# Kernel optimization log

Hardware: AMD Instinct MI355X
Metric: run time of the kernel (lower is better)

## Reference

```python
import jax, jax.numpy as jnp
import numpy as np
from jax import lax

DIM = 192
HEADS = 8
B, H, W = 8, 128, 128


def dwconv3x3(x, w):
    # x: [B,C,H,W], w: [C,1,3,3] depthwise (groups=C)
    return lax.conv_general_dilated(
        x, w, window_strides=(1, 1), padding='SAME',
        feature_group_count=x.shape[1],
        dimension_numbers=('NCHW', 'OIHW', 'NCHW'))


def conv1x1(x, w, b=None):
    # w: [Cout, Cin]
    y = jnp.einsum('oc,bchw->bohw', w, x)
    if b is not None:
        y = y + b[None, :, None, None]
    return y


def setup_inputs() -> dict:
    key = jax.random.key(0)
    ks = jax.random.split(key, 9)
    s = 0.02
    return {
        'x': jax.random.normal(ks[0], (B, DIM, H, W), jnp.float32),
        'w_qkv': jax.random.normal(ks[1], (3 * DIM, DIM), jnp.float32) * s,
        'b_qkv': jnp.zeros((3 * DIM,), jnp.float32),
        'w_dw': jax.random.normal(ks[2], (3 * DIM, 1, 3, 3), jnp.float32) * s,
        'b_dw': jnp.zeros((3 * DIM,), jnp.float32),
        'w_proj': jax.random.normal(ks[3], (DIM, DIM), jnp.float32) * s,
        'b_proj': jnp.zeros((DIM,), jnp.float32),
        'w_pos1': jax.random.normal(ks[4], (DIM, 1, 3, 3), jnp.float32) * s,
        'w_pos2': jax.random.normal(ks[5], (DIM, 1, 3, 3), jnp.float32) * s,
        'temperature': jnp.ones((HEADS, 1, 1), jnp.float32),
    }


def reference(x, w_qkv, b_qkv, w_dw, b_dw, w_proj, b_proj, w_pos1, w_pos2, temperature):
    b, c, h, w = x.shape
    heads = HEADS
    ch = c // heads

    qkv = conv1x1(x, w_qkv, b_qkv)
    qkv = dwconv3x3(qkv, w_dw) + b_dw[None, :, None, None]
    q_inp, k_inp, v_inp = jnp.split(qkv, 3, axis=1)

    def to_heads(t):  # [B,C,H,W] -> [B,heads,ch,HW]
        return t.reshape(b, heads, ch, h * w)

    q = to_heads(q_inp)
    k = to_heads(k_inp)
    v = to_heads(v_inp)

    # L2 normalize over hw (torch F.normalize, eps=1e-12)
    q = q / jnp.maximum(jnp.linalg.norm(q, axis=-1, keepdims=True), 1e-12)
    k = k / jnp.maximum(jnp.linalg.norm(k, axis=-1, keepdims=True), 1e-12)

    attn = jnp.einsum('bhce,bhde->bhcd', q, k) * temperature  # [B,heads,ch,ch]
    attn = jax.nn.softmax(attn, axis=-1)
    out = jnp.einsum('bhcd,bhde->bhce', attn, v)  # [B,heads,ch,HW]
    out = out.reshape(b, c, h, w)

    out = conv1x1(out, w_proj, b_proj)

    pos = dwconv3x3(v_inp, w_pos1)
    pos = jax.nn.gelu(pos, approximate=False)
    pos = dwconv3x3(pos, w_pos2)

    return out + pos
```

## Files before the change

### kernel.cpp

```cpp
#include <hip/hip_runtime.h>
#include <stdint.h>
#include <stddef.h>

#define NB 8
#define CC 192
#define C3 576
#define HGT 128
#define WID 128
#define HW 16384
#define NH 8

typedef short bf16x8 __attribute__((ext_vector_type(8)));
typedef float f32x4 __attribute__((ext_vector_type(4)));

__device__ __forceinline__ unsigned short f2bf(float f) {
  unsigned int u = __float_as_uint(f);
  u += 0x7fffu + ((u >> 16) & 1u);
  return (unsigned short)(u >> 16);
}
__device__ __forceinline__ float bf2f(unsigned short h) {
  return __uint_as_float(((unsigned int)h) << 16);
}
__device__ __forceinline__ unsigned int pk2(float a, float b) {
  return (unsigned int)f2bf(a) | ((unsigned int)f2bf(b) << 16);
}
__device__ __forceinline__ void gl_lds16(const void* g, void* l) {
  __builtin_amdgcn_global_load_lds(
      (const __attribute__((address_space(1))) unsigned int*)(uintptr_t)g,
      (__attribute__((address_space(3))) unsigned int*)(uint32_t)(uintptr_t)l,
      16, 0, 0);
}
__device__ __forceinline__ int xcd_swz(int g, int n) {
  return (g & 7) * (n >> 3) + (g >> 3);
}

__global__ __launch_bounds__(256) void ktrans(const float* __restrict__ x,
                                              unsigned char* __restrict__ xT) {
  __shared__ __align__(16) float lx[192 * 68];
  int wg = xcd_swz(blockIdx.x, gridDim.x);
  int pt = wg & 255, b = wg >> 8;
  int p0 = pt * 64;
  int tid = threadIdx.x;
#pragma unroll
  for (int i = 0; i < 12; ++i) {
    int f = tid + i * 256;
    int ic = f >> 4, q = f & 15;
    float4 v = *(const float4*)(x + ((size_t)(b * CC + ic)) * HW + p0 + q * 4);
    *(float4*)(lx + ic * 68 + q * 4) = v;
  }
  __syncthreads();
#pragma unroll
  for (int i = 0; i < 6; ++i) {
    int f = i * 256 + tid;
    int s = f >> 6, p = f & 63;
    unsigned int wv[4];
#pragma unroll
    for (int j = 0; j < 4; ++j)
      wv[j] = pk2(lx[(s * 8 + 2 * j) * 68 + p], lx[(s * 8 + 2 * j + 1) * 68 + p]);
    uint4 st; st.x = wv[0]; st.y = wv[1]; st.z = wv[2]; st.w = wv[3];
    *(uint4*)(xT + (((size_t)(b * 24 + s)) * HW + p0 + p) * 16) = st;
  }
}

__global__ void kwprep(const float* __restrict__ wq, unsigned char* __restrict__ wb) {
  int f = blockIdx.x * 256 + threadIdx.x;
  if (f >= C3 * 24) return;
  int oc = f / 24, s = f % 24;
  unsigned int wv[4];
#pragma unroll
  for (int j = 0; j < 4; ++j)
    wv[j] = pk2(wq[oc * 192 + s * 8 + 2 * j], wq[oc * 192 + s * 8 + 2 * j + 1]);
  uint4 st; st.x = wv[0]; st.y = wv[1]; st.z = wv[2]; st.w = wv[3];
  *(uint4*)(wb + (size_t)oc * 384 + ((s ^ (oc & 7)) * 16)) = st;
}

__global__ __launch_bounds__(256) void kconv1(const unsigned char* __restrict__ xT,
                                              const unsigned char* __restrict__ wb,
                                              const float* __restrict__ bqkv,
                                              unsigned short* __restrict__ t) {
  __shared__ __align__(16) unsigned char lds[73728];
  int wg = xcd_swz(blockIdx.x, gridDim.x);
  int ot = wg % 9;
  int pt = (wg / 9) & 127;
  int b = wg / 1152;
  int tid = threadIdx.x;
  const unsigned char* gB = wb + (size_t)ot * 64 * 384;
#pragma unroll
  for (int i = 0; i < 12; ++i) {
    int u2 = i * 256 + tid;
    int slot = u2 >> 7, px = u2 & 127;
    gl_lds16(xT + (((size_t)(b * 24 + slot)) * HW + pt * 128 + px) * 16, lds + u2 * 16);
  }
#pragma unroll
  for (int i = 0; i < 6; ++i)
    gl_lds16(gB + i * 4096 + tid * 16, lds + 49152 + i * 4096 + tid * 16);
  asm volatile("s_waitcnt vmcnt(0)" ::: "memory");
  __syncthreads();

  int lane = tid & 63, wv = tid >> 6;
  int l15 = lane & 15, gq = lane >> 4;
  int pw = (wv >> 1) * 64, ow = (wv & 1) * 32;
  f32x4 acc[4][2];
#pragma unroll
  for (int a = 0; a < 4; ++a)
#pragma unroll
    for (int c = 0; c < 2; ++c) acc[a][c] = (f32x4){0.f, 0.f, 0.f, 0.f};

#pragma unroll
  for (int kk = 0; kk < 6; ++kk) {
    int cb = kk * 64 + gq * 16;
    bf16x8 af[4], bfr[2];
#pragma unroll
    for (int mf = 0; mf < 4; ++mf)
      af[mf] = *(const bf16x8*)(lds + (((kk * 4 + gq) << 7) + pw + mf * 16 + l15) * 16);
#pragma unroll
    for (int nf = 0; nf < 2; ++nf) {
      int r = ow + nf * 16 + l15;
      bfr[nf] = *(const bf16x8*)(lds + 49152 + r * 384 + (cb ^ ((r & 7) << 4)));
    }
#pragma unroll
    for (int mf = 0; mf < 4; ++mf)
#pragma unroll
      for (int nf = 0; nf < 2; ++nf)
        acc[mf][nf] = __builtin_amdgcn_mfma_f32_16x16x32_bf16(af[mf], bfr[nf], acc[mf][nf], 0, 0, 0);
  }
#pragma unroll
  for (int nf = 0; nf < 2; ++nf) {
    int oc = ot * 64 + ow + nf * 16 + l15;
    float bias = bqkv[oc];
    int part = oc / 192, c = oc % 192;
    size_t rowb = ((size_t)((part * 8 + b) * CC + c)) * HW;
#pragma unroll
    for (int mf = 0; mf < 4; ++mf) {
      int p = pt * 128 + pw + mf * 16 + gq * 4;
      uint2 st;
      st.x = pk2(acc[mf][nf][0] + bias, acc[mf][nf][1] + bias);
      st.y = pk2(acc[mf][nf][2] + bias, acc[mf][nf][3] + bias);
      *(uint2*)(t + rowb + p) = st;
    }
  }
}

__global__ __launch_bounds__(256) void kdw(const unsigned short* __restrict__ src,
                                           const float* __restrict__ wdw,
                                           const float* __restrict__ bdw,
                                           int part, int mode,
                                           unsigned short* __restrict__ dst,
                                           float* __restrict__ nrm,
                                           unsigned char* __restrict__ vT) {
  __shared__ __align__(16) unsigned int smem[8 * 721];
  int wg = xcd_swz(blockIdx.x, gridDim.x);
  int cg = wg % 24, rt = (wg / 24) & 15, b = wg / 384;
  int y0 = rt * 8, chg0 = cg * 8;
  int tid = threadIdx.x;
  for (int i = tid; i < 5768; i += 256) smem[i] = 0;
  __syncthreads();
#pragma unroll
  for (int i = 0; i < 5; ++i) {
    int f = i * 256 + tid;
    int ch = f / 160, rem = f % 160;
    int r = rem >> 4, seg = rem & 15;
    int y = y0 - 1 + r;
    if (y >= 0 && y < HGT) {
      uint4 v = *(const uint4*)(src + ((size_t)(b * CC + chg0 + ch)) * HW + y * WID + seg * 8);
      unsigned int* dp = smem + ch * 721 + r * 72 + 4 + seg * 4;
      dp[0] = v.x; dp[1] = v.y; dp[2] = v.z; dp[3] = v.w;
    }
  }
  __syncthreads();

  int ch = tid >> 5, u = tid & 31;
  int row = u >> 2, xs = (u & 3) * 32;
  int gch = part * CC + chg0 + ch;
  float wv[9];
#pragma unroll
  for (int j = 0; j < 9; ++j) wv[j] = wdw[gch * 9 + j];
  float bias = bdw[gch];
  float outv[32];
  const unsigned int* tb = smem + ch * 721;
#pragma unroll
  for (int g = 0; g < 4; ++g) {
    int x0 = xs + g * 8;
    float v[3][12];
#pragma unroll
    for (int dy = 0; dy < 3; ++dy) {
      const unsigned int* rp = tb + (row + dy) * 72 + ((x0 + 6) >> 1);
#pragma unroll
      for (int m = 0; m < 6; ++m) {
        unsigned int w2 = rp[m];
        v[dy][2 * m] = bf2f((unsigned short)(w2 & 0xffff));
        v[dy][2 * m + 1] = bf2f((unsigned short)(w2 >> 16));
      }
    }
#pragma unroll
    for (int j = 0; j < 8; ++j) {
      float a = bias;
#pragma unroll
      for (int dy = 0; dy < 3; ++dy)
#pragma unroll
        for (int dx = 0; dx < 3; ++dx)
          a += v[dy][j + dx + 1] * wv[dy * 3 + dx];
      outv[g * 8 + j] = a;
    }
  }

  if (mode == 0) {
    size_t rb = ((size_t)(b * CC + chg0 + ch)) * HW + (size_t)(y0 + row) * WID + xs;
#pragma unroll
    for (int g = 0; g < 4; ++g) {
      uint4 st;
      st.x = pk2(outv[g * 8 + 0], outv[g * 8 + 1]);
      st.y = pk2(outv[g * 8 + 2], outv[g * 8 + 3]);
      st.z = pk2(outv[g * 8 + 4], outv[g * 8 + 5]);
      st.w = pk2(outv[g * 8 + 6], outv[g * 8 + 7]);
      *(uint4*)(dst + rb + g * 8) = st;
    }
    float s = 0.f;
#pragma unroll
    for (int i = 0; i < 32; ++i) s += outv[i] * outv[i];
#pragma unroll
    for (int m = 16; m >= 1; m >>= 1) s += __shfl_xor(s, m, 32);
    if (u == 0) {
      int qc = chg0 + ch;
      atomicAdd(nrm + (b * NH + qc / 24) * 24 + (qc % 24), s);
    }
  } else {
    __syncthreads();
    unsigned short* vt = (unsigned short*)smem;
#pragma unroll
    for (int g = 0; g < 4; ++g)
#pragma unroll
      for (int j = 0; j < 8; j += 2) {
        int x = xs + g * 8 + j;
        ((unsigned int*)smem)[ch * 512 + row * 64 + (x >> 1)] =
            pk2(outv[g * 8 + j], outv[g * 8 + j + 1]);
      }
    __syncthreads();
#pragma unroll
    for (int i = 0; i < 4; ++i) {
      int f = i * 256 + tid;
      int r = f >> 7, col = f & 127;
      unsigned int wvp[4];
#pragma unroll
      for (int e = 0; e < 4; ++e) {
        unsigned short a = vt[(2 * e) * 1024 + r * 128 + col];
        unsigned short bb = vt[(2 * e + 1) * 1024 + r * 128 + col];
        wvp[e] = (unsigned int)a | ((unsigned int)bb << 16);
      }
      uint4 st; st.x = wvp[0]; st.y = wvp[1]; st.z = wvp[2]; st.w = wvp[3];
      *(uint4*)(vT + (((size_t)(b * 24 + cg)) * HW + (size_t)(y0 + r) * WID + col) * 16) = st;
    }
  }
}

__global__ __launch_bounds__(256) void kgram(const unsigned short* __restrict__ q,
                                             const unsigned short* __restrict__ k,
                                             float* __restrict__ G) {
  __shared__ __align__(16) unsigned char qt[32768];
  __shared__ __align__(16) unsigned char kt[32768];
  __shared__ float gpart[4][32][32];
  int blk = blockIdx.x;
  int b = blk >> 5, h = (blk >> 2) & 7, qr = blk & 3;
  int tid = threadIdx.x, lane = tid & 63, w = tid >> 6;
  int l15 = lane & 15, gq = lane >> 4;
  for (int i = tid; i < 2048; i += 256) {
    ((unsigned int*)(qt + 24576))[i] = 0;
    ((unsigned int*)(kt + 24576))[i] = 0;
  }
  f32x4 acc[2][2];
#pragma unroll
  for (int a = 0; a < 2; ++a)
#pragma unroll
    for (int d = 0; d < 2; ++d) acc[a][d] = (f32x4){0.f, 0.f, 0.f, 0.f};
  for (int c = 0; c < 8; ++c) {
    __syncthreads();
    int px0 = qr * 4096 + c * 512;
#pragma unroll
    for (int i = 0; i < 6; ++i) {
      int f = i * 256 + tid;
      int rowc = f >> 6, seg = f & 63;
      size_t gofs = ((size_t)(b * CC + h * 24 + rowc)) * HW + px0 + seg * 8;
      unsigned int lofs = rowc * 1024 + ((seg * 16) ^ ((rowc & 7) << 4));
      *(uint4*)(qt + lofs) = *(const uint4*)(q + gofs);
      *(uint4*)(kt + lofs) = *(const uint4*)(k + gofs);
    }
    __syncthreads();
#pragma unroll
    for (int j = 0; j < 4; ++j) {
      int kk = w * 4 + j;
      int cb = kk * 64 + gq * 16;
      bf16x8 aq[2], bk[2];
#pragma unroll
      for (int ct = 0; ct < 2; ++ct) {
        int r = ct * 16 + l15;
        aq[ct] = *(const bf16x8*)(qt + r * 1024 + (cb ^ ((r & 7) << 4)));
        bk[ct] = *(const bf16x8*)(kt + r * 1024 + (cb ^ ((r & 7) << 4)));
      }
#pragma unroll
      for (int ct = 0; ct < 2; ++ct)
#pragma unroll
        for (int dt = 0; dt < 2; ++dt)
          acc[ct][dt] = __builtin_amdgcn_mfma_f32_16x16x32_bf16(aq[ct], bk[dt], acc[ct][dt], 0, 0, 0);
    }
  }
  __syncthreads();
#pragma unroll
  for (int ct = 0; ct < 2; ++ct)
#pragma unroll
    for (int dt = 0; dt < 2; ++dt)
#pragma unroll
      for (int r = 0; r < 4; ++r)
        gpart[w][ct * 16 + gq * 4 + r][dt * 16 + l15] = acc[ct][dt][r];
  __syncthreads();
  for (int f = tid; f < 576; f += 256) {
    int cc2 = f / 24, d = f % 24;
    float s = gpart[0][cc2][d] + gpart[1][cc2][d] + gpart[2][cc2][d] + gpart[3][cc2][d];
    atomicAdd(G + ((size_t)(b * NH + h)) * 576 + cc2 * 24 + d, s);
  }
}

__global__ __launch_bounds__(256) void kattn(const float* __restrict__ G,
                                             const float* __restrict__ nq,
                                             const float* __restrict__ nk,
                                             const float* __restrict__ temp,
                                             const float* __restrict__ wproj,
                                             unsigned char* __restrict__ W2) {
  __shared__ float attn[24][24];
  __shared__ float iq[24], ik[24];
  int bh = blockIdx.x;
  int h = bh & 7, b = bh >> 3;
  int tid = threadIdx.x;
  const float* Gb = G + (size_t)bh * 576;
  if (tid < 24) { float n = sqrtf(nq[bh * 24 + tid]); iq[tid] = 1.f / fmaxf(n, 1e-12f); }
  else if (tid < 48) { float n = sqrtf(nk[bh * 24 + tid - 24]); ik[tid - 24] = 1.f / fmaxf(n, 1e-12f); }
  __syncthreads();
  if (tid < 24) {
    float tmp = temp[h];
    float row[24];
    float mx = -1e30f;
#pragma unroll
    for (int d = 0; d < 24; ++d) {
      row[d] = Gb[tid * 24 + d] * iq[tid] * ik[d] * tmp;
      mx = fmaxf(mx, row[d]);
    }
    float sum = 0.f;
#pragma unroll
    for (int d = 0; d < 24; ++d) { float e = expf(row[d] - mx); row[d] = e; sum += e; }
    float inv = 1.f / sum;
#pragma unroll
    for (int d = 0; d < 24; ++d) attn[tid][d] = row[d] * inv;
  }
  __syncthreads();
  for (int i = 0; i < 18; ++i) {
    int f = tid + i * 256;
    if (f >= 4608) break;
    int oc = f / 24, d = f % 24;
    float s = 0.f;
#pragma unroll
    for (int c = 0; c < 24; ++c) s += wproj[oc * 192 + h * 24 + c] * attn[c][d];
    int gg = h * 24 + d;
    *(unsigned short*)(W2 + ((size_t)b * CC + oc) * 384 + ((gg * 2) ^ ((oc & 7) << 4))) = f2bf(s);
  }
}

__global__ __launch_bounds__(256) void kpos(const unsigned char* __restrict__ vT,
                                            const float* __restrict__ w1,
                                            const float* __restrict__ w2,
                                            unsigned short* __restrict__ pos) {
  __shared__ unsigned int vbuf[8 * 865];
  __shared__ unsigned int d1[8 * 721];
  int wg = xcd_swz(blockIdx.x, gridDim.x);
  int cg = wg % 24, rt = (wg / 24) & 15, b = wg / 384;
  int y0 = rt * 8, g0 = cg * 8;
  int tid = threadIdx.x;
  for (int i = tid; i < 6920; i += 256) vbuf[i] = 0;
  __syncthreads();
#pragma unroll
  for (int i = 0; i < 3; ++i) {
    int f = i * 256 + tid;
    int r = f >> 6, colp = f & 63;
    int y = y0 - 2 + r;
    if (y >= 0 && y < HGT) {
      const unsigned char* base = vT + (((size_t)(b * 24 + cg)) * HW + (size_t)y * WID + colp * 2) * 16;
      uint4 va = *(const uint4*)(base);
      uint4 vb2 = *(const uint4*)(base + 16);
      unsigned int la[4] = {va.x, va.y, va.z, va.w};
      unsigned int lb[4] = {vb2.x, vb2.y, vb2.z, vb2.w};
#pragma unroll
      for (int e = 0; e < 8; ++e) {
        unsigned int a16 = (la[e >> 1] >> ((e & 1) * 16)) & 0xffff;
        unsigned int b16 = (lb[e >> 1] >> ((e & 1) * 16)) & 0xffff;
        vbuf[e * 865 + r * 72 + colp + 4] = a16 | (b16 << 16);
      }
    }
  }
  __syncthreads();
  int ch = tid >> 5, u = tid & 31;
  {
    const float* wp = w1 + (g0 + ch) * 9;
    float wl[9];
#pragma unroll
    for (int j = 0; j < 9; ++j) wl[j] = wp[j];
    int x0 = u * 4;
    for (int rr = 0; rr < 10; ++rr) {
      int y = y0 - 1 + rr;
      unsigned int o0 = 0, o1 = 0;
      if (y >= 0 && y < HGT) {
        float v[3][8];
#pragma unroll
        for (int dy = 0; dy < 3; ++dy) {
          const unsigned int* rp = vbuf + ch * 865 + (rr + dy) * 72 + ((x0 + 6) >> 1);
#pragma unroll
          for (int m = 0; m < 4; ++m) {
            unsigned int w2r = rp[m];
            v[dy][2 * m] = bf2f((unsigned short)(w2r & 0xffff));
            v[dy][2 * m + 1] = bf2f((unsigned short)(w2r >> 16));
          }
        }
        float g4[4];
#pragma unroll
        for (int j = 0; j < 4; ++j) {
          float a = 0.f;
#pragma unroll
          for (int dy = 0; dy < 3; ++dy)
#pragma unroll
            for (int dx = 0; dx < 3; ++dx)
              a += v[dy][j + dx + 1] * wl[dy * 3 + dx];
          g4[j] = 0.5f * a * (1.f + erff(a * 0.70710678118f));
        }
        o0 = pk2(g4[0], g4[1]);
        o1 = pk2(g4[2], g4[3]);
      }
      unsigned int* dp = d1 + ch * 721 + rr * 72 + ((x0 + 8) >> 1);
      dp[0] = o0; dp[1] = o1;
    }
  }
  if (tid < 160) {
    int ech = tid / 20, rem = tid % 20;
    int rr = rem >> 1, side = rem & 1;
    int x = side ? 128 : -1;
    int y = y0 - 1 + rr;
    unsigned short val = 0;
    if (y >= 0 && y < HGT) {
      const float* wp = w1 + (g0 + ech) * 9;
      float a = 0.f;
      const unsigned short* vb16 = (const unsigned short*)(vbuf + ech * 865);
#pragma unroll
      for (int dy = 0; dy < 3; ++dy)
#pragma unroll
        for (int dx = 0; dx < 3; ++dx)
          a += bf2f(vb16[(rr + dy) * 144 + (x + dx + 7)]) * wp[dy * 3 + dx];
      val = f2bf(0.5f * a * (1.f + erff(a * 0.70710678118f)));
    }
    ((unsigned short*)(d1 + ech * 721))[rr * 144 + (x + 8)] = val;
  }
  __syncthreads();
  {
    const float* wp = w2 + (g0 + ch) * 9;
    float wl[9];
#pragma unroll
    for (int j = 0; j < 9; ++j) wl[j] = wp[j];
    int row = u >> 2, xs = (u & 3) * 32;
    size_t rb = ((size_t)(b * CC + g0 + ch)) * HW + (size_t)(y0 + row) * WID;
#pragma unroll
    for (int g = 0; g < 4; ++g) {
      int x0 = xs + g * 8;
      float v[3][12];
#pragma unroll
      for (int dy = 0; dy < 3; ++dy) {
        const unsigned int* rp = d1 + ch * 721 + (row + dy) * 72 + ((x0 + 6) >> 1);
#pragma unroll
        for (int m = 0; m < 6; ++m) {
          unsigned int w2r = rp[m];
          v[dy][2 * m] = bf2f((unsigned short)(w2r & 0xffff));
          v[dy][2 * m + 1] = bf2f((unsigned short)(w2r >> 16));
        }
      }
      uint4 st;
      float o[8];
#pragma unroll
      for (int j = 0; j < 8; ++j) {
        float a = 0.f;
#pragma unroll
        for (int dy = 0; dy < 3; ++dy)
#pragma unroll
          for (int dx = 0; dx < 3; ++dx)
            a += v[dy][j + dx + 1] * wl[dy * 3 + dx];
        o[j] = a;
      }
      st.x = pk2(o[0], o[1]); st.y = pk2(o[2], o[3]);
      st.z = pk2(o[4], o[5]); st.w = pk2(o[6], o[7]);
      *(uint4*)(pos + rb + x0) = st;
    }
  }
}

__global__ __launch_bounds__(256) void kproj(const unsigned char* __restrict__ vT,
                                             const unsigned char* __restrict__ W2,
                                             const float* __restrict__ bproj,
                                             const unsigned short* __restrict__ pos,
                                             float* __restrict__ out) {
  __shared__ __align__(16) unsigned char lds[73728];
  int wg = xcd_swz(blockIdx.x, gridDim.x);
  int ot = wg % 3;
  int pt = (wg / 3) & 127;
  int b = wg / 384;
  int tid = threadIdx.x;
  const unsigned char* gB = W2 + ((size_t)(b * CC + ot * 64)) * 384;
#pragma unroll
  for (int i = 0; i < 12; ++i) {
    int u2 = i * 256 + tid;
    int slot = u2 >> 7, px = u2 & 127;
    gl_lds16(vT + (((size_t)(b * 24 + slot)) * HW + pt * 128 + px) * 16, lds + u2 * 16);
  }
#pragma unroll
  for (int i = 0; i < 6; ++i)
    gl_lds16(gB + i * 4096 + tid * 16, lds + 49152 + i * 4096 + tid * 16);
  asm volatile("s_waitcnt vmcnt(0)" ::: "memory");
  __syncthreads();

  int lane = tid & 63, wv = tid >> 6;
  int l15 = lane & 15, gq = lane >> 4;
  int pw = (wv >> 1) * 64, ow = (wv & 1) * 32;
  f32x4 acc[4][2];
#pragma unroll
  for (int a = 0; a < 4; ++a)
#pragma unroll
    for (int c = 0; c < 2; ++c) acc[a][c] = (f32x4){0.f, 0.f, 0.f, 0.f};

#pragma unroll
  for (int kk = 0; kk < 6; ++kk) {
    int cb = kk * 64 + gq * 16;
    bf16x8 af[4], bfr[2];
#pragma unroll
    for (int mf = 0; mf < 4; ++mf)
      af[mf] = *(const bf16x8*)(lds + (((kk * 4 + gq) << 7) + pw + mf * 16 + l15) * 16);
#pragma unroll
    for (int nf = 0; nf < 2; ++nf) {
      int r = ow + nf * 16 + l15;
      bfr[nf] = *(const bf16x8*)(lds + 49152 + r * 384 + (cb ^ ((r & 7) << 4)));
    }
#pragma unroll
    for (int mf = 0; mf < 4; ++mf)
#pragma unroll
      for (int nf = 0; nf < 2; ++nf)
        acc[mf][nf] = __builtin_amdgcn_mfma_f32_16x16x32_bf16(af[mf], bfr[nf], acc[mf][nf], 0, 0, 0);
  }
#pragma unroll
  for (int nf = 0; nf < 2; ++nf) {
    int oc = ot * 64 + ow + nf * 16 + l15;
    float bias = bproj[oc];
    size_t rowb = ((size_t)(b * CC + oc)) * HW;
#pragma unroll
    for (int mf = 0; mf < 4; ++mf) {
      int p = pt * 128 + pw + mf * 16 + gq * 4;
      uint2 pv = *(const uint2*)(pos + rowb + p);
      float4 o;
      o.x = acc[mf][nf][0] + bias + bf2f((unsigned short)(pv.x & 0xffff));
      o.y = acc[mf][nf][1] + bias + bf2f((unsigned short)(pv.x >> 16));
      o.z = acc[mf][nf][2] + bias + bf2f((unsigned short)(pv.y & 0xffff));
      o.w = acc[mf][nf][3] + bias + bf2f((unsigned short)(pv.y >> 16));
      *(float4*)(out + rowb + p) = o;
    }
  }
}

#define OFF_W   ((size_t)0)
#define OFF_G   ((size_t)221184)
#define OFF_NQ  ((size_t)368640)
#define OFF_NK  ((size_t)374784)
#define OFF_W2  ((size_t)380928)
#define OFF_T   ((size_t)970752)
#define OFF_XT  ((size_t)151965696)

#define PART_ELEMS ((size_t)8 * CC * HW)

extern "C" void kernel_launch(void* const* d_in, const int* in_sizes, int n_in,
                              void* d_out, int out_size, void* d_ws, size_t ws_size,
                              hipStream_t stream) {
  const float* x     = (const float*)d_in[0];
  const float* wqkv  = (const float*)d_in[1];
  const float* bqkv  = (const float*)d_in[2];
  const float* wdw   = (const float*)d_in[3];
  const float* bdw   = (const float*)d_in[4];
  const float* wproj = (const float*)d_in[5];
  const float* bproj = (const float*)d_in[6];
  const float* wpos1 = (const float*)d_in[7];
  const float* wpos2 = (const float*)d_in[8];
  const float* temp  = (const float*)d_in[9];
  unsigned char* ws = (unsigned char*)d_ws;
  unsigned short* t = (unsigned short*)(ws + OFF_T);

  hipMemsetAsync(ws + OFF_G, 0, 147456 + 6144 + 6144, stream);
  kwprep<<<54, 256, 0, stream>>>(wqkv, ws + OFF_W);
  ktrans<<<2048, 256, 0, stream>>>(x, ws + OFF_XT);
  kconv1<<<9216, 256, 0, stream>>>(ws + OFF_XT, ws + OFF_W, bqkv, t);
  kdw<<<3072, 256, 0, stream>>>(t + 2 * PART_ELEMS, wdw, bdw, 2, 1,
                                nullptr, nullptr, ws + OFF_XT);
  kdw<<<3072, 256, 0, stream>>>(t, wdw, bdw, 0, 0,
                                t + 2 * PART_ELEMS, (float*)(ws + OFF_NQ), nullptr);
  kdw<<<3072, 256, 0, stream>>>(t + PART_ELEMS, wdw, bdw, 1, 0,
                                t, (float*)(ws + OFF_NK), nullptr);
  kgram<<<256, 256, 0, stream>>>(t + 2 * PART_ELEMS, t, (float*)(ws + OFF_G));
  kattn<<<64, 256, 0, stream>>>((const float*)(ws + OFF_G), (const float*)(ws + OFF_NQ),
                                (const float*)(ws + OFF_NK), temp, wproj, ws + OFF_W2);
  kpos<<<3072, 256, 0, stream>>>(ws + OFF_XT, wpos1, wpos2, t + PART_ELEMS);
  kproj<<<3072, 256, 0, stream>>>(ws + OFF_XT, ws + OFF_W2, bproj,
                                  t + PART_ELEMS, (float*)d_out);
}
```

Before: 352.0 us.

## Fuse q/k depthwise conv with Gram computation and pipeline the 1x1 GEMMs

The qkv 1x1 conv now writes q and k in a head-blocked, channel-interleaved layout. A new kernel fuses the q/k depthwise 3x3, the L2-norm accumulation and the q·k^T Gram MFMA, so the two intermediate q/k tensors no longer round-trip through memory. The v depthwise runs as its own kernel. Both the conv1 and proj GEMM kernels now loop over four 64-pixel tiles with double-buffered LDS prefetch and reuse the weights, using half as many blocks. The cost is heavier per-block work in the fused kernel, with redundant halo loads and atomics on G.

```diff
diff --git a/kernel.cpp b/kernel.cpp
--- a/kernel.cpp
+++ b/kernel.cpp
@@ -77,77 +77,251 @@
 __global__ __launch_bounds__(256) void kconv1(const unsigned char* __restrict__ xT,
                                               const unsigned char* __restrict__ wb,
                                               const float* __restrict__ bqkv,
-                                              unsigned short* __restrict__ t) {
+                                              unsigned short* __restrict__ vout,
+                                              unsigned char* __restrict__ qkout) {
   __shared__ __align__(16) unsigned char lds[73728];
   int wg = xcd_swz(blockIdx.x, gridDim.x);
-  int ot = wg % 9;
-  int pt = (wg / 9) & 127;
-  int b = wg / 1152;
+  int ot = wg % 9; int rest = wg / 9; int grp = rest & 63; int b = rest >> 6;
   int tid = threadIdx.x;
-  const unsigned char* gB = wb + (size_t)ot * 64 * 384;
-#pragma unroll
-  for (int i = 0; i < 12; ++i) {
-    int u2 = i * 256 + tid;
-    int slot = u2 >> 7, px = u2 & 127;
-    gl_lds16(xT + (((size_t)(b * 24 + slot)) * HW + pt * 128 + px) * 16, lds + u2 * 16);
-  }
+  const unsigned char* gB = wb + (size_t)ot * 24576;
 #pragma unroll
   for (int i = 0; i < 6; ++i)
     gl_lds16(gB + i * 4096 + tid * 16, lds + 49152 + i * 4096 + tid * 16);
-  asm volatile("s_waitcnt vmcnt(0)" ::: "memory");
-  __syncthreads();
-
-  int lane = tid & 63, wv = tid >> 6;
+  const unsigned char* gA = xT + (size_t)b * 24 * HW * 16;
+  int t0 = grp * 4;
+  {
+    int p0 = t0 * 64;
+#pragma unroll
+    for (int i = 0; i < 6; ++i) {
+      int f = i * 256 + tid;
+      gl_lds16(gA + (((size_t)(f >> 6)) * HW + p0 + (f & 63)) * 16, lds + f * 16);
+    }
+  }
+  int lane = tid & 63, w = tid >> 6;
   int l15 = lane & 15, gq = lane >> 4;
-  int pw = (wv >> 1) * 64, ow = (wv & 1) * 32;
-  f32x4 acc[4][2];
-#pragma unroll
-  for (int a = 0; a < 4; ++a)
-#pragma unroll
-    for (int c = 0; c < 2; ++c) acc[a][c] = (f32x4){0.f, 0.f, 0.f, 0.f};
-
-#pragma unroll
-  for (int kk = 0; kk < 6; ++kk) {
-    int cb = kk * 64 + gq * 16;
-    bf16x8 af[4], bfr[2];
-#pragma unroll
-    for (int mf = 0; mf < 4; ++mf)
-      af[mf] = *(const bf16x8*)(lds + (((kk * 4 + gq) << 7) + pw + mf * 16 + l15) * 16);
-#pragma unroll
-    for (int nf = 0; nf < 2; ++nf) {
-      int r = ow + nf * 16 + l15;
-      bfr[nf] = *(const bf16x8*)(lds + 49152 + r * 384 + (cb ^ ((r & 7) << 4)));
-    }
-#pragma unroll
-    for (int mf = 0; mf < 4; ++mf)
-#pragma unroll
-      for (int nf = 0; nf < 2; ++nf)
-        acc[mf][nf] = __builtin_amdgcn_mfma_f32_16x16x32_bf16(af[mf], bfr[nf], acc[mf][nf], 0, 0, 0);
-  }
-#pragma unroll
-  for (int nf = 0; nf < 2; ++nf) {
-    int oc = ot * 64 + ow + nf * 16 + l15;
-    float bias = bqkv[oc];
-    int part = oc / 192, c = oc % 192;
-    size_t rowb = ((size_t)((part * 8 + b) * CC + c)) * HW;
-#pragma unroll
-    for (int mf = 0; mf < 4; ++mf) {
-      int p = pt * 128 + pw + mf * 16 + gq * 4;
+  int pw = w * 16;
+  float bias[4];
+  size_t obase[4];
+  int isv[4];
+#pragma unroll
+  for (int nf = 0; nf < 4; ++nf) {
+    int oc = ot * 64 + nf * 16 + l15;
+    bias[nf] = bqkv[oc];
+    if (oc >= 384) {
+      isv[nf] = 1;
+      obase[nf] = ((size_t)(b * CC + oc - 384)) * HW * 2;
+    } else {
+      isv[nf] = 0;
+      int part = oc >= 192 ? 1 : 0;
+      int cm = oc - part * 192;
+      int h = cm / 24, ch = cm % 24;
+      obase[nf] = (size_t)(((part * 8 + b) * 8 + h) * 128) * 6144 + ch * 16 + (gq & 1) * 8;
+    }
+  }
+  for (int it = 0; it < 4; ++it) {
+    int tile = t0 + it;
+    asm volatile("s_waitcnt vmcnt(0)" ::: "memory");
+    __syncthreads();
+    int nb = it & 1;
+    if (it < 3) {
+      int p1 = (tile + 1) * 64;
+#pragma unroll
+      for (int i = 0; i < 6; ++i) {
+        int f = i * 256 + tid;
+        gl_lds16(gA + (((size_t)(f >> 6)) * HW + p1 + (f & 63)) * 16,
+                 lds + ((nb ^ 1) * 24576) + f * 16);
+      }
+    }
+    f32x4 acc[4];
+#pragma unroll
+    for (int nf = 0; nf < 4; ++nf) acc[nf] = (f32x4){0.f, 0.f, 0.f, 0.f};
+#pragma unroll
+    for (int kk = 0; kk < 6; ++kk) {
+      bf16x8 a = *(const bf16x8*)(lds + nb * 24576 + ((((kk * 4 + gq) << 6) + pw + l15) * 16));
+      int cb = kk * 64 + gq * 16;
+#pragma unroll
+      for (int nf = 0; nf < 4; ++nf) {
+        int r = nf * 16 + l15;
+        bf16x8 bfr = *(const bf16x8*)(lds + 49152 + r * 384 + (cb ^ ((r & 7) << 4)));
+        acc[nf] = __builtin_amdgcn_mfma_f32_16x16x32_bf16(a, bfr, acc[nf], 0, 0, 0);
+      }
+    }
+    int p = tile * 64 + pw + gq * 4;
+    int y = p >> 7, x = p & 127;
+#pragma unroll
+    for (int nf = 0; nf < 4; ++nf) {
       uint2 st;
-      st.x = pk2(acc[mf][nf][0] + bias, acc[mf][nf][1] + bias);
-      st.y = pk2(acc[mf][nf][2] + bias, acc[mf][nf][3] + bias);
-      *(uint2*)(t + rowb + p) = st;
-    }
-  }
-}
-
-__global__ __launch_bounds__(256) void kdw(const unsigned short* __restrict__ src,
+      st.x = pk2(acc[nf][0] + bias[nf], acc[nf][1] + bias[nf]);
+      st.y = pk2(acc[nf][2] + bias[nf], acc[nf][3] + bias[nf]);
+      if (isv[nf]) {
+        *(uint2*)((unsigned char*)vout + obase[nf] + (size_t)p * 2) = st;
+      } else {
+        *(uint2*)(qkout + obase[nf] + (size_t)y * 6144 + (x >> 3) * 384) = st;
+      }
+    }
+  }
+}
+
+__device__ __forceinline__ void dwoct(const unsigned char* lds, int t, int r0,
+                                      int xu, int ch, const float* w, float bias,
+                                      float* o) {
+#pragma unroll
+  for (int j = 0; j < 8; ++j) o[j] = bias;
+#pragma unroll
+  for (int dy = 0; dy < 3; ++dy) {
+    int ub = ((t * 6 + r0 + dy) * 16) * 24 + ch;
+    union { bf16x8 v; unsigned short s[8]; } m;
+    m.v = *(const bf16x8*)(lds + (size_t)(ub + xu * 24) * 16);
+    unsigned short lft = *(const unsigned short*)(lds + (size_t)(ub + (xu > 0 ? xu - 1 : 0) * 24) * 16 + 14);
+    unsigned short rgt = *(const unsigned short*)(lds + (size_t)(ub + (xu < 15 ? xu + 1 : 15) * 24) * 16);
+    float vwin[10];
+    vwin[0] = (xu > 0) ? bf2f(lft) : 0.f;
+    vwin[9] = (xu < 15) ? bf2f(rgt) : 0.f;
+#pragma unroll
+    for (int j = 0; j < 8; ++j) vwin[1 + j] = bf2f(m.s[j]);
+#pragma unroll
+    for (int j = 0; j < 8; ++j)
+      o[j] += vwin[j] * w[dy * 3] + vwin[j + 1] * w[dy * 3 + 1] + vwin[j + 2] * w[dy * 3 + 2];
+  }
+}
+
+__global__ __launch_bounds__(256) void kqk(const unsigned char* __restrict__ qk,
                                            const float* __restrict__ wdw,
                                            const float* __restrict__ bdw,
-                                           int part, int mode,
-                                           unsigned short* __restrict__ dst,
-                                           float* __restrict__ nrm,
-                                           unsigned char* __restrict__ vT) {
+                                           float* __restrict__ G,
+                                           float* __restrict__ nq,
+                                           float* __restrict__ nk) {
+  __shared__ __align__(16) unsigned char lds[73728];
+  int wg = xcd_swz(blockIdx.x, gridDim.x);
+  int band = wg & 31, bh = wg >> 5;
+  int h = bh & 7, b = bh >> 3;
+  int y0 = band * 4;
+  int tid = threadIdx.x;
+  if (band == 0 || band == 31) {
+#pragma unroll
+    for (int i = 0; i < 18; ++i)
+      *(uint4*)(lds + (i * 256 + tid) * 16) = (uint4){0, 0, 0, 0};
+    __syncthreads();
+  }
+#pragma unroll
+  for (int i = 0; i < 18; ++i) {
+    int f = i * 256 + tid;
+    int t = f / 2304, rem = f % 2304;
+    int r = rem / 384, u = rem % 384;
+    int y = y0 - 1 + r;
+    if (y >= 0 && y < HGT)
+      gl_lds16(qk + ((size_t)(((t * 8 + b) * 8 + h) * 128 + y)) * 6144 + u * 16,
+               lds + f * 16);
+  }
+  asm volatile("s_waitcnt vmcnt(0)" ::: "memory");
+  __syncthreads();
+
+  int lane = tid & 63, w = tid >> 6;
+  int l15 = lane & 15, gq = lane >> 4;
+  int ch0 = l15;
+  int ch1 = (l15 < 8) ? 16 + l15 : 23;
+  int c0 = h * 24 + ch0, c1 = h * 24 + ch1;
+  float wq0[9], wq1[9], wk0[9], wk1[9];
+#pragma unroll
+  for (int j = 0; j < 9; ++j) {
+    wq0[j] = wdw[c0 * 9 + j];        wq1[j] = wdw[c1 * 9 + j];
+    wk0[j] = wdw[(192 + c0) * 9 + j]; wk1[j] = wdw[(192 + c1) * 9 + j];
+  }
+  float bq0 = bdw[c0], bq1 = bdw[c1], bk0 = bdw[192 + c0], bk1 = bdw[192 + c1];
+
+  f32x4 acc[2][2];
+#pragma unroll
+  for (int ct = 0; ct < 2; ++ct)
+#pragma unroll
+    for (int dt = 0; dt < 2; ++dt) acc[ct][dt] = (f32x4){0.f, 0.f, 0.f, 0.f};
+  float nq0 = 0.f, nq1 = 0.f, nk0 = 0.f, nk1 = 0.f;
+
+#pragma unroll
+  for (int j4 = 0; j4 < 4; ++j4) {
+    int kt = w * 4 + j4;
+    int r0 = kt >> 2;
+    int xu = (kt & 3) * 4 + gq;
+    union { bf16x8 v; unsigned int u[4]; } fq0, fq1, fk0, fk1;
+    {
+      float o[8];
+      dwoct(lds, 0, r0, xu, ch0, wq0, bq0, o);
+#pragma unroll
+      for (int j = 0; j < 8; ++j) nq0 += o[j] * o[j];
+#pragma unroll
+      for (int e = 0; e < 4; ++e) fq0.u[e] = pk2(o[2 * e], o[2 * e + 1]);
+    }
+    {
+      float o[8];
+      dwoct(lds, 0, r0, xu, ch1, wq1, bq1, o);
+#pragma unroll
+      for (int j = 0; j < 8; ++j) nq1 += o[j] * o[j];
+#pragma unroll
+      for (int e = 0; e < 4; ++e) fq1.u[e] = pk2(o[2 * e], o[2 * e + 1]);
+    }
+    {
+      float o[8];
+      dwoct(lds, 1, r0, xu, ch0, wk0, bk0, o);
+#pragma unroll
+      for (int j = 0; j < 8; ++j) nk0 += o[j] * o[j];
+#pragma unroll
+      for (int e = 0; e < 4; ++e) fk0.u[e] = pk2(o[2 * e], o[2 * e + 1]);
+    }
+    {
+      float o[8];
+      dwoct(lds, 1, r0, xu, ch1, wk1, bk1, o);
+#pragma unroll
+      for (int j = 0; j < 8; ++j) nk1 += o[j] * o[j];
+#pragma unroll
+      for (int e = 0; e < 4; ++e) fk1.u[e] = pk2(o[2 * e], o[2 * e + 1]);
+    }
+    acc[0][0] = __builtin_amdgcn_mfma_f32_16x16x32_bf16(fq0.v, fk0.v, acc[0][0], 0, 0, 0);
+    acc[0][1] = __builtin_amdgcn_mfma_f32_16x16x32_bf16(fq0.v, fk1.v, acc[0][1], 0, 0, 0);
+    acc[1][0] = __builtin_amdgcn_mfma_f32_16x16x32_bf16(fq1.v, fk0.v, acc[1][0], 0, 0, 0);
+    acc[1][1] = __builtin_amdgcn_mfma_f32_16x16x32_bf16(fq1.v, fk1.v, acc[1][1], 0, 0, 0);
+  }
+  __syncthreads();
+  float* gp = (float*)lds;
+#pragma unroll
+  for (int ct = 0; ct < 2; ++ct)
+#pragma unroll
+    for (int dt = 0; dt < 2; ++dt)
+      *(f32x4*)(gp + (((w * 4 + ct * 2 + dt) * 64) + lane) * 4) = acc[ct][dt];
+  nq0 += __shfl_xor(nq0, 16); nq0 += __shfl_xor(nq0, 32);
+  nq1 += __shfl_xor(nq1, 16); nq1 += __shfl_xor(nq1, 32);
+  nk0 += __shfl_xor(nk0, 16); nk0 += __shfl_xor(nk0, 32);
+  nk1 += __shfl_xor(nk1, 16); nk1 += __shfl_xor(nk1, 32);
+  int nb24 = (b * NH + h) * 24;
+  if (lane < 16) {
+    atomicAdd(nq + nb24 + l15, nq0);
+    atomicAdd(nk + nb24 + l15, nk0);
+  }
+  if (lane < 8) {
+    atomicAdd(nq + nb24 + 16 + l15, nq1);
+    atomicAdd(nk + nb24 + 16 + l15, nk1);
+  }
+  __syncthreads();
+  float* Gb = G + (size_t)(b * NH + h) * 576;
+#pragma unroll
+  for (int ii = 0; ii < 3; ++ii) {
+    int f = ii * 256 + tid;
+    if (f < 576) {
+      int c = f / 24, d = f % 24;
+      int t4 = ((c >> 4) << 1) + (d >> 4);
+      int lane16 = (d & 15) + (((c & 15) >> 2) << 4);
+      int reg = c & 3;
+      float s = 0.f;
+#pragma unroll
+      for (int w4 = 0; w4 < 4; ++w4)
+        s += gp[((w4 * 4 + t4) * 64 + lane16) * 4 + reg];
+      atomicAdd(Gb + f, s);
+    }
+  }
+}
+
+__global__ __launch_bounds__(256) void kdwv(const unsigned short* __restrict__ src,
+                                            const float* __restrict__ wdw,
+                                            const float* __restrict__ bdw,
+                                            unsigned char* __restrict__ vT) {
   __shared__ __align__(16) unsigned int smem[8 * 721];
   int wg = xcd_swz(blockIdx.x, gridDim.x);
   int cg = wg % 24, rt = (wg / 24) & 15, b = wg / 384;
@@ -168,10 +342,9 @@
     }
   }
   __syncthreads();
-
   int ch = tid >> 5, u = tid & 31;
   int row = u >> 2, xs = (u & 3) * 32;
-  int gch = part * CC + chg0 + ch;
+  int gch = 384 + chg0 + ch;
   float wv[9];
 #pragma unroll
   for (int j = 0; j < 9; ++j) wv[j] = wdw[gch * 9 + j];
@@ -203,119 +376,30 @@
       outv[g * 8 + j] = a;
     }
   }
-
-  if (mode == 0) {
-    size_t rb = ((size_t)(b * CC + chg0 + ch)) * HW + (size_t)(y0 + row) * WID + xs;
-#pragma unroll
-    for (int g = 0; g < 4; ++g) {
-      uint4 st;
-      st.x = pk2(outv[g * 8 + 0], outv[g * 8 + 1]);
-      st.y = pk2(outv[g * 8 + 2], outv[g * 8 + 3]);
-      st.z = pk2(outv[g * 8 + 4], outv[g * 8 + 5]);
-      st.w = pk2(outv[g * 8 + 6], outv[g * 8 + 7]);
-      *(uint4*)(dst + rb + g * 8) = st;
-    }
-    float s = 0.f;
-#pragma unroll
-    for (int i = 0; i < 32; ++i) s += outv[i] * outv[i];
-#pragma unroll
-    for (int m = 16; m >= 1; m >>= 1) s += __shfl_xor(s, m, 32);
-    if (u == 0) {
-      int qc = chg0 + ch;
-      atomicAdd(nrm + (b * NH + qc / 24) * 24 + (qc % 24), s);
-    }
-  } else {
-    __syncthreads();
-    unsigned short* vt = (unsigned short*)smem;
-#pragma unroll
-    for (int g = 0; g < 4; ++g)
-#pragma unroll
-      for (int j = 0; j < 8; j += 2) {
-        int x = xs + g * 8 + j;
-        ((unsigned int*)smem)[ch * 512 + row * 64 + (x >> 1)] =
-            pk2(outv[g * 8 + j], outv[g * 8 + j + 1]);
-      }
-    __syncthreads();
-#pragma unroll
-    for (int i = 0; i < 4; ++i) {
-      int f = i * 256 + tid;
-      int r = f >> 7, col = f & 127;
-      unsigned int wvp[4];
-#pragma unroll
-      for (int e = 0; e < 4; ++e) {
-        unsigned short a = vt[(2 * e) * 1024 + r * 128 + col];
-        unsigned short bb = vt[(2 * e + 1) * 1024 + r * 128 + col];
-        wvp[e] = (unsigned int)a | ((unsigned int)bb << 16);
-      }
-      uint4 st; st.x = wvp[0]; st.y = wvp[1]; st.z = wvp[2]; st.w = wvp[3];
-      *(uint4*)(vT + (((size_t)(b * 24 + cg)) * HW + (size_t)(y0 + r) * WID + col) * 16) = st;
-    }
-  }
-}
-
-__global__ __launch_bounds__(256) void kgram(const unsigned short* __restrict__ q,
-                                             const unsigned short* __restrict__ k,
-                                             float* __restrict__ G) {
-  __shared__ __align__(16) unsigned char qt[32768];
-  __shared__ __align__(16) unsigned char kt[32768];
-  __shared__ float gpart[4][32][32];
-  int blk = blockIdx.x;
-  int b = blk >> 5, h = (blk >> 2) & 7, qr = blk & 3;
-  int tid = threadIdx.x, lane = tid & 63, w = tid >> 6;
-  int l15 = lane & 15, gq = lane >> 4;
-  for (int i = tid; i < 2048; i += 256) {
-    ((unsigned int*)(qt + 24576))[i] = 0;
-    ((unsigned int*)(kt + 24576))[i] = 0;
-  }
-  f32x4 acc[2][2];
-#pragma unroll
-  for (int a = 0; a < 2; ++a)
-#pragma unroll
-    for (int d = 0; d < 2; ++d) acc[a][d] = (f32x4){0.f, 0.f, 0.f, 0.f};
-  for (int c = 0; c < 8; ++c) {
-    __syncthreads();
-    int px0 = qr * 4096 + c * 512;
-#pragma unroll
-    for (int i = 0; i < 6; ++i) {
-      int f = i * 256 + tid;
-      int rowc = f >> 6, seg = f & 63;
-      size_t gofs = ((size_t)(b * CC + h * 24 + rowc)) * HW + px0 + seg * 8;
-      unsigned int lofs = rowc * 1024 + ((seg * 16) ^ ((rowc & 7) << 4));
-      *(uint4*)(qt + lofs) = *(const uint4*)(q + gofs);
-      *(uint4*)(kt + lofs) = *(const uint4*)(k + gofs);
-    }
-    __syncthreads();
-#pragma unroll
-    for (int j = 0; j < 4; ++j) {
-      int kk = w * 4 + j;
-      int cb = kk * 64 + gq * 16;
-      bf16x8 aq[2], bk[2];
-#pragma unroll
-      for (int ct = 0; ct < 2; ++ct) {
-        int r = ct * 16 + l15;
-        aq[ct] = *(const bf16x8*)(qt + r * 1024 + (cb ^ ((r & 7) << 4)));
-        bk[ct] = *(const bf16x8*)(kt + r * 1024 + (cb ^ ((r & 7) << 4)));
-      }
-#pragma unroll
-      for (int ct = 0; ct < 2; ++ct)
-#pragma unroll
-        for (int dt = 0; dt < 2; ++dt)
-          acc[ct][dt] = __builtin_amdgcn_mfma_f32_16x16x32_bf16(aq[ct], bk[dt], acc[ct][dt], 0, 0, 0);
-    }
-  }
-  __syncthreads();
-#pragma unroll
-  for (int ct = 0; ct < 2; ++ct)
-#pragma unroll
-    for (int dt = 0; dt < 2; ++dt)
-#pragma unroll
-      for (int r = 0; r < 4; ++r)
-        gpart[w][ct * 16 + gq * 4 + r][dt * 16 + l15] = acc[ct][dt][r];
-  __syncthreads();
-  for (int f = tid; f < 576; f += 256) {
-    int cc2 = f / 24, d = f % 24;
-    float s = gpart[0][cc2][d] + gpart[1][cc2][d] + gpart[2][cc2][d] + gpart[3][cc2][d];
-    atomicAdd(G + ((size_t)(b * NH + h)) * 576 + cc2 * 24 + d, s);
+  __syncthreads();
+  unsigned short* vt = (unsigned short*)smem;
+#pragma unroll
+  for (int g = 0; g < 4; ++g)
+#pragma unroll
+    for (int j = 0; j < 8; j += 2) {
+      int x = xs + g * 8 + j;
+      ((unsigned int*)smem)[ch * 512 + row * 64 + (x >> 1)] =
+          pk2(outv[g * 8 + j], outv[g * 8 + j + 1]);
+    }
+  __syncthreads();
+#pragma unroll
+  for (int i = 0; i < 4; ++i) {
+    int f = i * 256 + tid;
+    int r = f >> 7, col = f & 127;
+    unsigned int wvp[4];
+#pragma unroll
+    for (int e = 0; e < 4; ++e) {
+      unsigned short a = vt[(2 * e) * 1024 + r * 128 + col];
+      unsigned short bb = vt[(2 * e + 1) * 1024 + r * 128 + col];
+      wvp[e] = (unsigned int)a | ((unsigned int)bb << 16);
+    }
+    uint4 st; st.x = wvp[0]; st.y = wvp[1]; st.z = wvp[2]; st.w = wvp[3];
+    *(uint4*)(vT + (((size_t)(b * 24 + cg)) * HW + (size_t)(y0 + r) * WID + col) * 16) = st;
   }
 }
 
@@ -502,65 +586,71 @@
                                              float* __restrict__ out) {
   __shared__ __align__(16) unsigned char lds[73728];
   int wg = xcd_swz(blockIdx.x, gridDim.x);
-  int ot = wg % 3;
-  int pt = (wg / 3) & 127;
-  int b = wg / 384;
+  int ot = wg % 3; int rest = wg / 3; int grp = rest & 63; int b = rest >> 6;
   int tid = threadIdx.x;
-  const unsigned char* gB = W2 + ((size_t)(b * CC + ot * 64)) * 384;
-#pragma unroll
-  for (int i = 0; i < 12; ++i) {
-    int u2 = i * 256 + tid;
-    int slot = u2 >> 7, px = u2 & 127;
-    gl_lds16(vT + (((size_t)(b * 24 + slot)) * HW + pt * 128 + px) * 16, lds + u2 * 16);
-  }
+  const unsigned char* gB = W2 + ((size_t)(b * 192 + ot * 64)) * 384;
 #pragma unroll
   for (int i = 0; i < 6; ++i)
     gl_lds16(gB + i * 4096 + tid * 16, lds + 49152 + i * 4096 + tid * 16);
-  asm volatile("s_waitcnt vmcnt(0)" ::: "memory");
-  __syncthreads();
-
-  int lane = tid & 63, wv = tid >> 6;
+  const unsigned char* gA = vT + (size_t)b * 24 * HW * 16;
+  int t0 = grp * 4;
+  {
+    int p0 = t0 * 64;
+#pragma unroll
+    for (int i = 0; i < 6; ++i) {
+      int f = i * 256 + tid;
+      gl_lds16(gA + (((size_t)(f >> 6)) * HW + p0 + (f & 63)) * 16, lds + f * 16);
+    }
+  }
+  int lane = tid & 63, w = tid >> 6;
   int l15 = lane & 15, gq = lane >> 4;
-  int pw = (wv >> 1) * 64, ow = (wv & 1) * 32;
-  f32x4 acc[4][2];
-#pragma unroll
-  for (int a = 0; a < 4; ++a)
-#pragma unroll
-    for (int c = 0; c < 2; ++c) acc[a][c] = (f32x4){0.f, 0.f, 0.f, 0.f};
-
-#pragma unroll
-  for (int kk = 0; kk < 6; ++kk) {
-    int cb = kk * 64 + gq * 16;
-    bf16x8 af[4], bfr[2];
-#pragma unroll
-    for (int mf = 0; mf < 4; ++mf)
-      af[mf] = *(const bf16x8*)(lds + (((kk * 4 + gq) << 7) + pw + mf * 16 + l15) * 16);
-#pragma unroll
-    for (int nf = 0; nf < 2; ++nf) {
-      int r = ow + nf * 16 + l15;
-      bfr[nf] = *(const bf16x8*)(lds + 49152 + r * 384 + (cb ^ ((r & 7) << 4)));
-    }
-#pragma unroll
-    for (int mf = 0; mf < 4; ++mf)
-#pragma unroll
-      for (int nf = 0; nf < 2; ++nf)
-        acc[mf][nf] = __builtin_amdgcn_mfma_f32_16x16x32_bf16(af[mf], bfr[nf], acc[mf][nf], 0, 0, 0);
-  }
-#pragma unroll
-  for (int nf = 0; nf < 2; ++nf) {
-    int oc = ot * 64 + ow + nf * 16 + l15;
-    float bias = bproj[oc];
-    size_t rowb = ((size_t)(b * CC + oc)) * HW;
-#pragma unroll
-    for (int mf = 0; mf < 4; ++mf) {
-      int p = pt * 128 + pw + mf * 16 + gq * 4;
-      uint2 pv = *(const uint2*)(pos + rowb + p);
+  int pw = w * 16;
+  float bias[4];
+  size_t obase[4];
+#pragma unroll
+  for (int nf = 0; nf < 4; ++nf) {
+    int oc = ot * 64 + nf * 16 + l15;
+    bias[nf] = bproj[oc];
+    obase[nf] = ((size_t)(b * 192 + oc)) * HW;
+  }
+  for (int it = 0; it < 4; ++it) {
+    int tile = t0 + it;
+    asm volatile("s_waitcnt vmcnt(0)" ::: "memory");
+    __syncthreads();
+    int nb = it & 1;
+    if (it < 3) {
+      int p1 = (tile + 1) * 64;
+#pragma unroll
+      for (int i = 0; i < 6; ++i) {
+        int f = i * 256 + tid;
+        gl_lds16(gA + (((size_t)(f >> 6)) * HW + p1 + (f & 63)) * 16,
+                 lds + ((nb ^ 1) * 24576) + f * 16);
+      }
+    }
+    f32x4 acc[4];
+#pragma unroll
+    for (int nf = 0; nf < 4; ++nf) acc[nf] = (f32x4){0.f, 0.f, 0.f, 0.f};
+#pragma unroll
+    for (int kk = 0; kk < 6; ++kk) {
+      bf16x8 a = *(const bf16x8*)(lds + nb * 24576 + ((((kk * 4 + gq) << 6) + pw + l15) * 16));
+      int cb = kk * 64 + gq * 16;
+#pragma unroll
+      for (int nf = 0; nf < 4; ++nf) {
+        int r = nf * 16 + l15;
+        bf16x8 bfr = *(const bf16x8*)(lds + 49152 + r * 384 + (cb ^ ((r & 7) << 4)));
+        acc[nf] = __builtin_amdgcn_mfma_f32_16x16x32_bf16(a, bfr, acc[nf], 0, 0, 0);
+      }
+    }
+    int p = tile * 64 + pw + gq * 4;
+#pragma unroll
+    for (int nf = 0; nf < 4; ++nf) {
+      uint2 pv = *(const uint2*)(pos + obase[nf] + p);
       float4 o;
-      o.x = acc[mf][nf][0] + bias + bf2f((unsigned short)(pv.x & 0xffff));
-      o.y = acc[mf][nf][1] + bias + bf2f((unsigned short)(pv.x >> 16));
-      o.z = acc[mf][nf][2] + bias + bf2f((unsigned short)(pv.y & 0xffff));
-      o.w = acc[mf][nf][3] + bias + bf2f((unsigned short)(pv.y >> 16));
-      *(float4*)(out + rowb + p) = o;
+      o.x = acc[nf][0] + bias[nf] + bf2f((unsigned short)(pv.x & 0xffff));
+      o.y = acc[nf][1] + bias[nf] + bf2f((unsigned short)(pv.x >> 16));
+      o.z = acc[nf][2] + bias[nf] + bf2f((unsigned short)(pv.y & 0xffff));
+      o.w = acc[nf][3] + bias[nf] + bf2f((unsigned short)(pv.y >> 16));
+      *(float4*)(out + obase[nf] + p) = o;
     }
   }
 }
@@ -570,10 +660,9 @@
 #define OFF_NQ  ((size_t)368640)
 #define OFF_NK  ((size_t)374784)
 #define OFF_W2  ((size_t)380928)
-#define OFF_T   ((size_t)970752)
+#define OFF_QK  ((size_t)970752)
+#define OFF_V   ((size_t)101634048)
 #define OFF_XT  ((size_t)151965696)
-
-#define PART_ELEMS ((size_t)8 * CC * HW)
 
 extern "C" void kernel_launch(void* const* d_in, const int* in_sizes, int n_in,
                               void* d_out, int out_size, void* d_ws, size_t ws_size,
@@ -589,22 +678,20 @@
   const float* wpos2 = (const float*)d_in[8];
   const float* temp  = (const float*)d_in[9];
   unsigned char* ws = (unsigned char*)d_ws;
-  unsigned short* t = (unsigned short*)(ws + OFF_T);
 
   hipMemsetAsync(ws + OFF_G, 0, 147456 + 6144 + 6144, stream);
   kwprep<<<54, 256, 0, stream>>>(wqkv, ws + OFF_W);
   ktrans<<<2048, 256, 0, stream>>>(x, ws + OFF_XT);
-  kconv1<<<9216, 256, 0, stream>>>(ws + OFF_XT, ws + OFF_W, bqkv, t);
-  kdw<<<3072, 256, 0, stream>>>(t + 2 * PART_ELEMS, wdw, bdw, 2, 1,
-                                nullptr, nullptr, ws + OFF_XT);
-  kdw<<<3072, 256, 0, stream>>>(t, wdw, bdw, 0, 0,
-                                t + 2 * PART_ELEMS, (float*)(ws + OFF_NQ), nullptr);
-  kdw<<<3072, 256, 0, stream>>>(t + PART_ELEMS, wdw, bdw, 1, 0,
-                                t, (float*)(ws + OFF_NK), nullptr);
-  kgram<<<256, 256, 0, stream>>>(t + 2 * PART_ELEMS, t, (float*)(ws + OFF_G));
+  kconv1<<<4608, 256, 0, stream>>>(ws + OFF_XT, ws + OFF_W, bqkv,
+                                   (unsigned short*)(ws + OFF_V), ws + OFF_QK);
+  kqk<<<2048, 256, 0, stream>>>(ws + OFF_QK, wdw, bdw, (float*)(ws + OFF_G),
+                                (float*)(ws + OFF_NQ), (float*)(ws + OFF_NK));
+  kdwv<<<3072, 256, 0, stream>>>((const unsigned short*)(ws + OFF_V), wdw, bdw,
+                                 ws + OFF_XT);
   kattn<<<64, 256, 0, stream>>>((const float*)(ws + OFF_G), (const float*)(ws + OFF_NQ),
                                 (const float*)(ws + OFF_NK), temp, wproj, ws + OFF_W2);
-  kpos<<<3072, 256, 0, stream>>>(ws + OFF_XT, wpos1, wpos2, t + PART_ELEMS);
-  kproj<<<3072, 256, 0, stream>>>(ws + OFF_XT, ws + OFF_W2, bproj,
-                                  t + PART_ELEMS, (float*)d_out);
-}
+  kpos<<<3072, 256, 0, stream>>>(ws + OFF_XT, wpos1, wpos2,
+                                 (unsigned short*)(ws + OFF_QK));
+  kproj<<<1536, 256, 0, stream>>>(ws + OFF_XT, ws + OFF_W2, bproj,
+                                  (const unsigned short*)(ws + OFF_QK), (float*)d_out);
+}
```

Result: faster. 326.0 us (-7.4%).
